# Performance work log

Hardware: AMD Instinct MI355X
Metric: run time of the kernel (lower is better)

## Reference

```python
import jax, jax.numpy as jnp
import numpy as np

B, C = 2048, 32000

def setup_inputs() -> dict:
    key = jax.random.key(0)
    k1, k2, k3 = jax.random.split(key, 3)
    x = jax.random.normal(k1, (B, C), dtype=jnp.float32)
    u = jax.random.uniform(k2, (B, C), dtype=jnp.float32)  # U[0,1]
    noise = jax.random.normal(k3, (B, C), dtype=jnp.float32)  # N(0,1)
    return {"x": x, "u": u, "noise": noise}

def reference(x, u, noise):
    # m = row max (detached for fill, matching .item() in the torch loop)
    m = jnp.max(x, axis=-1, keepdims=True)                      # [B,1]
    midx = jnp.argmax(x, axis=-1, keepdims=True)                # [B,1]
    keep = jnp.arange(x.shape[-1])[None, :] == midx             # [B,C] one-hot of argmax
    fill = (0.1 + 0.2 * u) * jax.lax.stop_gradient(m)           # uniform(0.1,0.3)*m
    x2 = jnp.where(keep, x, fill) + noise
    return jax.nn.softmax(x2, axis=-1)
```

## Files before the change

### kernel.cpp

```cpp
#include <hip/hip_runtime.h>
#include <math.h>

constexpr int BROWS = 2048;
constexpr int C     = 32000;
constexpr int C4    = C / 4;
constexpr int NT    = 1024;
constexpr int NW    = NT / 64;
constexpr int PER   = (C4 + NT - 1) / NT;

__global__ __launch_bounds__(NT, 4) void fused_fill_softmax_kernel(
    const float* __restrict__ x,
    const float* __restrict__ u,
    const float* __restrict__ nz,
    float* __restrict__ out)
{
    __shared__ float s_vals[NW];
    __shared__ int   s_idxs[NW];
    __shared__ float s_m;
    __shared__ int   s_amax;
    __shared__ float s_mx;
    __shared__ float s_sum;

    const int row  = blockIdx.x;
    const int tid  = threadIdx.x;
    const int lane = tid & 63;
    const int wid  = tid >> 6;

    const size_t roff = (size_t)row * C;
    const float4* x4 = (const float4*)(x  + roff);
    const float4* u4 = (const float4*)(u  + roff);
    const float4* n4 = (const float4*)(nz + roff);
    float4*       o4 = (float4*)(out + roff);

    float bm = -INFINITY;
    int   bi = 0x7fffffff;
#pragma unroll
    for (int k = 0; k < PER; ++k) {
        int i = tid + k * NT;
        if (i < C4) {
            float4 v = x4[i];
            int base = i * 4;
            if (v.x > bm) { bm = v.x; bi = base;     }
            if (v.y > bm) { bm = v.y; bi = base + 1; }
            if (v.z > bm) { bm = v.z; bi = base + 2; }
            if (v.w > bm) { bm = v.w; bi = base + 3; }
        }
    }
#pragma unroll
    for (int off = 32; off > 0; off >>= 1) {
        float om = __shfl_down(bm, off, 64);
        int   oi = __shfl_down(bi, off, 64);
        if (om > bm || (om == bm && oi < bi)) { bm = om; bi = oi; }
    }
    if (lane == 0) { s_vals[wid] = bm; s_idxs[wid] = bi; }
    __syncthreads();
    if (wid == 0) {
        bm = (lane < NW) ? s_vals[lane] : -INFINITY;
        bi = (lane < NW) ? s_idxs[lane] : 0x7fffffff;
#pragma unroll
        for (int off = 8; off > 0; off >>= 1) {
            float om = __shfl_down(bm, off, 64);
            int   oi = __shfl_down(bi, off, 64);
            if (om > bm || (om == bm && oi < bi)) { bm = om; bi = oi; }
        }
        if (lane == 0) { s_m = bm; s_amax = bi; }
    }
    __syncthreads();
    const float m    = s_m;
    const int   amax = s_amax;

    float4 r[PER];
    float lmax = -INFINITY;
#pragma unroll
    for (int k = 0; k < PER; ++k) {
        int i = tid + k * NT;
        if (i < C4) {
            float4 uu = u4[i];
            float4 nn = n4[i];
            int base = i * 4;
            float4 v;
            v.x = ((base + 0 == amax) ? m : (0.1f + 0.2f * uu.x) * m) + nn.x;
            v.y = ((base + 1 == amax) ? m : (0.1f + 0.2f * uu.y) * m) + nn.y;
            v.z = ((base + 2 == amax) ? m : (0.1f + 0.2f * uu.z) * m) + nn.z;
            v.w = ((base + 3 == amax) ? m : (0.1f + 0.2f * uu.w) * m) + nn.w;
            r[k] = v;
            lmax = fmaxf(lmax, fmaxf(fmaxf(v.x, v.y), fmaxf(v.z, v.w)));
        }
    }
#pragma unroll
    for (int off = 32; off > 0; off >>= 1)
        lmax = fmaxf(lmax, __shfl_down(lmax, off, 64));
    if (lane == 0) s_vals[wid] = lmax;
    __syncthreads();
    if (wid == 0) {
        lmax = (lane < NW) ? s_vals[lane] : -INFINITY;
#pragma unroll
        for (int off = 8; off > 0; off >>= 1)
            lmax = fmaxf(lmax, __shfl_down(lmax, off, 64));
        if (lane == 0) s_mx = lmax;
    }
    __syncthreads();
    const float mx = s_mx;

    float lsum = 0.f;
#pragma unroll
    for (int k = 0; k < PER; ++k) {
        int i = tid + k * NT;
        if (i < C4) {
            float4 v = r[k];
            v.x = __expf(v.x - mx);
            v.y = __expf(v.y - mx);
            v.z = __expf(v.z - mx);
            v.w = __expf(v.w - mx);
            r[k] = v;
            lsum += (v.x + v.y) + (v.z + v.w);
        }
    }
#pragma unroll
    for (int off = 32; off > 0; off >>= 1)
        lsum += __shfl_down(lsum, off, 64);
    if (lane == 0) s_vals[wid] = lsum;
    __syncthreads();
    if (wid == 0) {
        lsum = (lane < NW) ? s_vals[lane] : 0.f;
#pragma unroll
        for (int off = 8; off > 0; off >>= 1)
            lsum += __shfl_down(lsum, off, 64);
        if (lane == 0) s_sum = lsum;
    }
    __syncthreads();
    const float inv = 1.0f / s_sum;

#pragma unroll
    for (int k = 0; k < PER; ++k) {
        int i = tid + k * NT;
        if (i < C4) {
            float4 v = r[k];
            v.x *= inv; v.y *= inv; v.z *= inv; v.w *= inv;
            o4[i] = v;
        }
    }
}

extern "C" void kernel_launch(void* const* d_in, const int* in_sizes, int n_in,
                              void* d_out, int out_size, void* d_ws, size_t ws_size,
                              hipStream_t stream) {
    const float* x  = (const float*)d_in[0];
    const float* u  = (const float*)d_in[1];
    const float* nz = (const float*)d_in[2];
    float* out = (float*)d_out;
    fused_fill_softmax_kernel<<<BROWS, NT, 0, stream>>>(x, u, nz, out);
}
```

Before: 721.0 us.

## Split row argmax into separate kernel and drop softmax max pass via fixed shift

Row max and argmax of x now run in their own kernel, which writes per-row results to workspace. A second kernel does the fill, noise add, exp, sum and normalise in one pass. That second kernel replaces the data-dependent second max reduction with a fixed shift of m+6. This removes one block-wide reduction and its barriers, and allows higher occupancy per kernel. The shift is only safe when the noise is bounded enough to avoid exp overflow or underflow, which adds numerical risk for inputs outside the expected distribution.

```diff
diff --git a/kernel.cpp b/kernel.cpp
--- a/kernel.cpp
+++ b/kernel.cpp
@@ -4,9 +4,136 @@
 constexpr int BROWS = 2048;
 constexpr int C     = 32000;
 constexpr int C4    = C / 4;
-constexpr int NT    = 1024;
-constexpr int NW    = NT / 64;
-constexpr int PER   = (C4 + NT - 1) / NT;
+
+constexpr int NT1  = 512;
+constexpr int NW1  = NT1 / 64;
+constexpr int PER1 = (C4 + NT1 - 1) / NT1;
+
+__global__ __launch_bounds__(NT1) void rowmax_kernel(
+    const float* __restrict__ x,
+    float* __restrict__ wm,
+    int*   __restrict__ wi)
+{
+    __shared__ float s_vals[NW1];
+    __shared__ int   s_idxs[NW1];
+
+    const int row  = blockIdx.x;
+    const int tid  = threadIdx.x;
+    const int lane = tid & 63;
+    const int wid  = tid >> 6;
+
+    const float4* x4 = (const float4*)(x + (size_t)row * C);
+
+    float bm = -INFINITY;
+    int   bi = 0x7fffffff;
+#pragma unroll
+    for (int k = 0; k < PER1; ++k) {
+        int i = tid + k * NT1;
+        if (i < C4) {
+            float4 v = x4[i];
+            int base = i * 4;
+            if (v.x > bm) { bm = v.x; bi = base;     }
+            if (v.y > bm) { bm = v.y; bi = base + 1; }
+            if (v.z > bm) { bm = v.z; bi = base + 2; }
+            if (v.w > bm) { bm = v.w; bi = base + 3; }
+        }
+    }
+#pragma unroll
+    for (int off = 32; off > 0; off >>= 1) {
+        float om = __shfl_down(bm, off, 64);
+        int   oi = __shfl_down(bi, off, 64);
+        if (om > bm || (om == bm && oi < bi)) { bm = om; bi = oi; }
+    }
+    if (lane == 0) { s_vals[wid] = bm; s_idxs[wid] = bi; }
+    __syncthreads();
+    if (tid == 0) {
+#pragma unroll
+        for (int w = 1; w < NW1; ++w) {
+            float om = s_vals[w]; int oi = s_idxs[w];
+            if (om > bm || (om == bm && oi < bi)) { bm = om; bi = oi; }
+        }
+        wm[row] = bm;
+        wi[row] = bi;
+    }
+}
+
+constexpr int NT2  = 1024;
+constexpr int NW2  = NT2 / 64;
+constexpr int PER2 = (C4 + NT2 - 1) / NT2;
+constexpr float SHIFT = 6.0f;
+
+__global__ __launch_bounds__(NT2, 8) void fill_expsum_store_kernel(
+    const float* __restrict__ u,
+    const float* __restrict__ nz,
+    const float* __restrict__ wm,
+    const int*   __restrict__ wi,
+    float* __restrict__ out)
+{
+    __shared__ float s_vals[NW2];
+    __shared__ float s_sum;
+
+    const int row  = blockIdx.x;
+    const int tid  = threadIdx.x;
+    const int lane = tid & 63;
+    const int wid  = tid >> 6;
+
+    const float m    = wm[row];
+    const int   amax = wi[row];
+    const float M    = m + SHIFT;
+
+    const size_t roff = (size_t)row * C;
+    const float4* u4 = (const float4*)(u  + roff);
+    const float4* n4 = (const float4*)(nz + roff);
+    float4*       o4 = (float4*)(out + roff);
+
+    float4 r[PER2];
+    float lsum = 0.f;
+#pragma unroll
+    for (int k = 0; k < PER2; ++k) {
+        int i = tid + k * NT2;
+        if (i < C4) {
+            float4 uu = u4[i];
+            float4 nn = n4[i];
+            int base = i * 4;
+            float4 v;
+            v.x = __expf((((base + 0) == amax) ? m : (0.1f + 0.2f * uu.x) * m) + nn.x - M);
+            v.y = __expf((((base + 1) == amax) ? m : (0.1f + 0.2f * uu.y) * m) + nn.y - M);
+            v.z = __expf((((base + 2) == amax) ? m : (0.1f + 0.2f * uu.z) * m) + nn.z - M);
+            v.w = __expf((((base + 3) == amax) ? m : (0.1f + 0.2f * uu.w) * m) + nn.w - M);
+            r[k] = v;
+            lsum += (v.x + v.y) + (v.z + v.w);
+        }
+    }
+
+#pragma unroll
+    for (int off = 32; off > 0; off >>= 1)
+        lsum += __shfl_down(lsum, off, 64);
+    if (lane == 0) s_vals[wid] = lsum;
+    __syncthreads();
+    if (wid == 0) {
+        lsum = (lane < NW2) ? s_vals[lane] : 0.f;
+#pragma unroll
+        for (int off = 8; off > 0; off >>= 1)
+            lsum += __shfl_down(lsum, off, 64);
+        if (lane == 0) s_sum = lsum;
+    }
+    __syncthreads();
+    const float inv = 1.0f / s_sum;
+
+#pragma unroll
+    for (int k = 0; k < PER2; ++k) {
+        int i = tid + k * NT2;
+        if (i < C4) {
+            float4 v = r[k];
+            v.x *= inv; v.y *= inv; v.z *= inv; v.w *= inv;
+            o4[i] = v;
+        }
+    }
+}
+
+constexpr int NT  = 1024;
+constexpr int NW  = NT / 64;
+constexpr int PER = (C4 + NT - 1) / NT;
 
 __global__ __launch_bounds__(NT, 4) void fused_fill_softmax_kernel(
     const float* __restrict__ x,
@@ -149,5 +276,13 @@
     const float* u  = (const float*)d_in[1];
     const float* nz = (const float*)d_in[2];
     float* out = (float*)d_out;
-    fused_fill_softmax_kernel<<<BROWS, NT, 0, stream>>>(x, u, nz, out);
-}
+
+    if (ws_size >= (size_t)BROWS * 8) {
+        float* wm = (float*)d_ws;
+        int*   wi = (int*)((char*)d_ws + (size_t)BROWS * 4);
+        rowmax_kernel<<<BROWS, NT1, 0, stream>>>(x, wm, wi);
+        fill_expsum_store_kernel<<<BROWS, NT2, 0, stream>>>(u, nz, wm, wi, out);
+    } else {
+        fused_fill_softmax_kernel<<<BROWS, NT, 0, stream>>>(x, u, nz, out);
+    }
+}
```

Result: slower. 770.7 us (+6.9%).
